# Kernel tuning notes

Measured on AMD Instinct MI355X. Metric: run time of the kernel, lower is better.

## Reference

```python
import jax, jax.numpy as jnp
import numpy as np

DIM = 2048
NH = 16
NKV = 4
HD = DIM // NH  # 128
ROPE_BASE = 10000.0
QK_GAIN_INIT = 1.0


def setup_inputs() -> dict:
    key = jax.random.key(0)
    ks = jax.random.split(key, 6)
    kv_dim = NKV * HD
    s = 0.02
    return {
        "x": jax.random.normal(ks[0], (2, 2048, DIM), dtype=jnp.float32),
        "wq": jax.random.normal(ks[1], (DIM, DIM), dtype=jnp.float32) * s,
        "wk": jax.random.normal(ks[2], (kv_dim, DIM), dtype=jnp.float32) * s,
        "wv": jax.random.normal(ks[3], (kv_dim, DIM), dtype=jnp.float32) * s,
        "wproj": jax.random.normal(ks[4], (DIM, DIM), dtype=jnp.float32) * s,
        "q_gain": jnp.full((NH,), QK_GAIN_INIT, dtype=jnp.float32),
    }


def _rms_norm(t):
    eps = jnp.asarray(jnp.finfo(t.dtype).eps, t.dtype)
    ms = jnp.mean(jnp.square(t), axis=-1, keepdims=True)
    return t * jax.lax.rsqrt(ms + eps)


def _rope_tables(seqlen, dtype):
    inv_freq = 1.0 / (ROPE_BASE ** (np.arange(0, HD, 2, dtype=np.float32) / HD))
    t = np.arange(seqlen, dtype=np.float32)
    freqs = np.outer(t, inv_freq)  # [S, HD/2]
    cos = jnp.asarray(np.cos(freqs), dtype=dtype)[None, None]  # [1,1,S,HD/2]
    sin = jnp.asarray(np.sin(freqs), dtype=dtype)[None, None]
    return cos, sin


def _apply_rotary(x, cos, sin):
    half = x.shape[-1] // 2
    x1, x2 = x[..., :half], x[..., half:]
    return jnp.concatenate((x1 * cos + x2 * sin, -x1 * sin + x2 * cos), axis=-1)


def reference(x, wq, wk, wv, wproj, q_gain):
    B, S, D = x.shape
    # projections (torch F.linear: x @ W.T), reshape to [B, H, S, HD]
    q = (x @ wq.T).reshape(B, S, NH, HD).transpose(0, 2, 1, 3)
    k = (x @ wk.T).reshape(B, S, NKV, HD).transpose(0, 2, 1, 3)
    v = (x @ wv.T).reshape(B, S, NKV, HD).transpose(0, 2, 1, 3)
    q = _rms_norm(q)
    k = _rms_norm(k)
    cos, sin = _rope_tables(S, q.dtype)
    q = _apply_rotary(q, cos, sin)
    k = _apply_rotary(k, cos, sin)
    q = q * q_gain.astype(q.dtype)[None, :, None, None]
    # GQA: expand kv heads
    G = NH // NKV
    k = jnp.repeat(k, G, axis=1)  # [B, NH, S, HD]
    v = jnp.repeat(v, G, axis=1)
    scale = 1.0 / np.sqrt(HD)
    scores = jnp.einsum("bhsd,bhtd->bhst", q, k) * scale
    causal = jnp.tril(jnp.ones((S, S), dtype=bool))
    scores = jnp.where(causal[None, None], scores, jnp.finfo(scores.dtype).min)
    attn = jax.nn.softmax(scores, axis=-1)
    y = jnp.einsum("bhst,bhtd->bhsd", attn, v)
    y = y.transpose(0, 2, 1, 3).reshape(B, S, D)
    return y @ wproj.T
```

## Files before the change

kernel.cpp:

```cpp
#include <hip/hip_runtime.h>
#include <hip/hip_bf16.h>
#include <stdint.h>

#define DIM 2048
#define NH 16
#define NKV 4
#define HD 128
#define BATCH 2
#define SEQ 2048

typedef unsigned short ushort_t;
typedef __attribute__((ext_vector_type(8))) short short8;
typedef __attribute__((ext_vector_type(4))) float f32x4;
typedef __attribute__((ext_vector_type(16))) float f32x16;

__device__ inline ushort_t f2b(float f) {
    union { float f; uint32_t u; } v; v.f = f;
    uint32_t r = (v.u + 0x7fffu + ((v.u >> 16) & 1u)) >> 16;
    return (ushort_t)r;
}

__device__ inline float fexp2(float x) {
#if __has_builtin(__builtin_amdgcn_exp2f)
    return __builtin_amdgcn_exp2f(x);
#else
    float r; asm("v_exp_f32 %0, %1" : "=v"(r) : "v"(x)); return r;
#endif
}

__device__ inline uint32_t pk2bf(float a, float b) {
    uint32_t r;
    asm("v_cvt_pk_bf16_f32 %0, %1, %2" : "=v"(r) : "v"(a), "v"(b));
    return r;
}

__global__ void cast_all(const float* __restrict__ x, const float* __restrict__ wq,
                         const float* __restrict__ wk, const float* __restrict__ wv,
                         const float* __restrict__ wp,
                         ushort_t* __restrict__ xb, ushort_t* __restrict__ wqkvb,
                         ushort_t* __restrict__ wprojb) {
    const int stride = gridDim.x * blockDim.x;
    for (int i = blockIdx.x * blockDim.x + threadIdx.x; i < 4718592; i += stride) {
        const float* s; ushort_t* d; int off;
        if (i < 2097152)      { s = x;  d = xb;               off = i; }
        else if (i < 3145728) { s = wq; d = wqkvb;            off = i - 2097152; }
        else if (i < 3407872) { s = wk; d = wqkvb + 4194304;  off = i - 3145728; }
        else if (i < 3670016) { s = wv; d = wqkvb + 5242880;  off = i - 3407872; }
        else                  { s = wp; d = wprojb;           off = i - 3670016; }
        float4 v = ((const float4*)s)[off];
        ushort4 o;
        o.x = f2b(v.x); o.y = f2b(v.y); o.z = f2b(v.z); o.w = f2b(v.w);
        ((ushort4*)d)[off] = o;
    }
}

__device__ inline void gload_lds16(const ushort_t* g, ushort_t* l) {
    __builtin_amdgcn_global_load_lds((const __attribute__((address_space(1))) void*)g,
                                     (__attribute__((address_space(3))) void*)l, 16, 0, 0);
}

__launch_bounds__(256, 2)
__global__ void gemm_bt(const ushort_t* __restrict__ A, const ushort_t* __restrict__ Bm,
                        float* __restrict__ C, int M, int N, int K) {
    __shared__ ushort_t lA[128 * 64];
    __shared__ ushort_t lB[128 * 64];
    const int t = threadIdx.x;
    const int lane = t & 63;
    const int w = t >> 6;
    const int wr = w >> 1, wc = w & 1;
    const int g = lane >> 4, l16 = lane & 15;
    const int nwg = gridDim.x * gridDim.y;
    const int bid = blockIdx.y * gridDim.x + blockIdx.x;
    const int cpx = nwg >> 3;
    const int swz = (bid & 7) * cpx + (bid >> 3);
    const int nbx = gridDim.x;
    const int m0 = (swz / nbx) * 128, n0 = (swz % nbx) * 128;

    f32x4 acc[4][4];
#pragma unroll
    for (int i = 0; i < 4; i++)
#pragma unroll
        for (int j = 0; j < 4; j++) acc[i][j] = (f32x4){0, 0, 0, 0};

    const int row_s = t >> 3;
    const int cx = t & 7;
    const int xr = (lane & 7);

    for (int kt = 0; kt < (K >> 6); ++kt) {
        const int k0 = kt * 64;
        __syncthreads();
#pragma unroll
        for (int i = 0; i < 4; i++) {
            const int ra = i * 32 + row_s;
            gload_lds16(A + (size_t)(m0 + ra) * K + k0 + ((cx ^ (row_s & 7)) * 8), lA + i * 2048 + t * 8);
            gload_lds16(Bm + (size_t)(n0 + ra) * K + k0 + ((cx ^ (row_s & 7)) * 8), lB + i * 2048 + t * 8);
        }
        __syncthreads();
#pragma unroll
        for (int kk = 0; kk < 2; kk++) {
            short8 af[4], bf[4];
#pragma unroll
            for (int i = 0; i < 4; i++) {
                af[i] = *(const short8*)(lA + (wr * 64 + i * 16 + l16) * 64 + (((kk * 4 + g) ^ xr) * 8));
                bf[i] = *(const short8*)(lB + (wc * 64 + i * 16 + l16) * 64 + (((kk * 4 + g) ^ xr) * 8));
            }
#pragma unroll
            for (int i = 0; i < 4; i++)
#pragma unroll
                for (int j = 0; j < 4; j++)
                    acc[i][j] = __builtin_amdgcn_mfma_f32_16x16x32_bf16(af[i], bf[j], acc[i][j], 0, 0, 0);
        }
    }
#pragma unroll
    for (int i = 0; i < 4; i++)
#pragma unroll
        for (int j = 0; j < 4; j++) {
            int rb = m0 + wr * 64 + i * 16 + g * 4;
            int cb = n0 + wc * 64 + j * 16 + l16;
#pragma unroll
            for (int r = 0; r < 4; r++)
                C[(size_t)(rb + r) * N + cb] = acc[i][j][r];
        }
}

__launch_bounds__(256, 2)
__global__ void gemm_qkv(const ushort_t* __restrict__ A, const ushort_t* __restrict__ Bm,
                         const float* __restrict__ qgain,
                         ushort_t* __restrict__ qb, ushort_t* __restrict__ kb,
                         ushort_t* __restrict__ vtb) {
    const int K = 2048;
    __shared__ ushort_t lA[128 * 64];
    __shared__ ushort_t lB[128 * 64];
    __shared__ float psum[2][128];
    const int t = threadIdx.x;
    const int lane = t & 63;
    const int w = t >> 6;
    const int wr = w >> 1, wc = w & 1;
    const int g = lane >> 4, l16 = lane & 15;
    const int nwg = gridDim.x * gridDim.y;
    const int bid = blockIdx.y * gridDim.x + blockIdx.x;
    const int cpx = nwg >> 3;
    const int swz = (bid & 7) * cpx + (bid >> 3);
    const int nt = swz % 24;
    const int m0 = (swz / 24) * 128, n0 = nt * 128;

    int cm[4];
    cm[0] = wc * 32 + l16;
    cm[1] = wc * 32 + 16 + l16;
    cm[2] = cm[0] + 64;
    cm[3] = cm[1] + 64;

    f32x4 acc[4][4];
#pragma unroll
    for (int i = 0; i < 4; i++)
#pragma unroll
        for (int j = 0; j < 4; j++) acc[i][j] = (f32x4){0, 0, 0, 0};

    const int row_s = t >> 3;
    const int cx = t & 7;
    const int xr = (lane & 7);

    for (int kt = 0; kt < (K >> 6); ++kt) {
        const int k0 = kt * 64;
        __syncthreads();
#pragma unroll
        for (int i = 0; i < 4; i++) {
            const int ra = i * 32 + row_s;
            gload_lds16(A + (size_t)(m0 + ra) * K + k0 + ((cx ^ (row_s & 7)) * 8), lA + i * 2048 + t * 8);
            gload_lds16(Bm + (size_t)(n0 + ra) * K + k0 + ((cx ^ (row_s & 7)) * 8), lB + i * 2048 + t * 8);
        }
        __syncthreads();
#pragma unroll
        for (int kk = 0; kk < 2; kk++) {
            short8 af[4], bf[4];
#pragma unroll
            for (int i = 0; i < 4; i++) {
                af[i] = *(const short8*)(lA + (wr * 64 + i * 16 + l16) * 64 + (((kk * 4 + g) ^ xr) * 8));
                bf[i] = *(const short8*)(lB + cm[i] * 64 + (((kk * 4 + g) ^ xr) * 8));
            }
#pragma unroll
            for (int i = 0; i < 4; i++)
#pragma unroll
                for (int j = 0; j < 4; j++)
                    acc[i][j] = __builtin_amdgcn_mfma_f32_16x16x32_bf16(af[i], bf[j], acc[i][j], 0, 0, 0);
        }
    }

    const int b = m0 >> 11;
    const int s0 = m0 & 2047;

    if (nt < 20) {
        float ssq[4][4];
#pragma unroll
        for (int i = 0; i < 4; i++)
#pragma unroll
            for (int r = 0; r < 4; r++) {
                float v = 0.0f;
#pragma unroll
                for (int j = 0; j < 4; j++) v += acc[i][j][r] * acc[i][j][r];
#pragma unroll
                for (int m = 1; m < 16; m <<= 1) v += __shfl_xor(v, m, 64);
                ssq[i][r] = v;
            }
        if (l16 == 0) {
#pragma unroll
            for (int i = 0; i < 4; i++)
#pragma unroll
                for (int r = 0; r < 4; r++)
                    psum[wc][wr * 64 + i * 16 + g * 4 + r] = ssq[i][r];
        }
        __syncthreads();

        const float gsc = (nt < 16) ? qgain[nt] * (0.08838834764831845f * 1.4426950408889634f)
                                    : 1.0f;
        ushort_t* outp = (nt < 16) ? qb + (size_t)(b * NH + nt) * SEQ * HD
                                   : kb + (size_t)(b * NKV + (nt - 16)) * SEQ * HD;
        const float inv0 = exp2f(-(float)cm[0] * (13.287712379549449f / 64.0f));
        const float inv1 = exp2f(-(float)cm[1] * (13.287712379549449f / 64.0f));
#pragma unroll
        for (int i = 0; i < 4; i++)
#pragma unroll
            for (int r = 0; r < 4; r++) {
                const int sloc = wr * 64 + i * 16 + g * 4 + r;
                const float tot = psum[0][sloc] + psum[1][sloc];
                const float rg = rsqrtf(tot * (1.0f / 128.0f) + 1.1920929e-07f) * gsc;
                const float fs = (float)(s0 + sloc);
                ushort_t* orow = outp + (size_t)(s0 + sloc) * HD;
#pragma unroll
                for (int jp = 0; jp < 2; jp++) {
                    float x1 = acc[i][jp][r], x2 = acc[i][jp + 2][r];
                    float sn, c;
                    __sincosf(fs * (jp ? inv1 : inv0), &sn, &c);
                    orow[cm[jp]]      = f2b((x1 * c + x2 * sn) * rg);
                    orow[cm[jp] + 64] = f2b((x2 * c - x1 * sn) * rg);
                }
            }
    } else {
        ushort_t* vout = vtb + (size_t)((b * NKV + (nt - 20)) * HD) * SEQ;
#pragma unroll
        for (int i = 0; i < 4; i++)
#pragma unroll
            for (int j = 0; j < 4; j++) {
                ushort4 o;
                o.x = f2b(acc[i][j][0]); o.y = f2b(acc[i][j][1]);
                o.z = f2b(acc[i][j][2]); o.w = f2b(acc[i][j][3]);
                *(ushort4*)(vout + (size_t)cm[j] * SEQ + s0 + wr * 64 + i * 16 + g * 4) = o;
            }
    }
}

#define KVB 64

__launch_bounds__(256, 2)
__global__ void attn(const ushort_t* __restrict__ qbuf, const ushort_t* __restrict__ kbuf,
                     const ushort_t* __restrict__ vtbuf, ushort_t* __restrict__ ybuf) {
    __shared__ ushort_t Klds[2][KVB * HD];
    __shared__ ushort_t Vlds[2][HD * KVB];

    const int idx = blockIdx.x;
    const int pass = idx >> 8;
    const int rr0 = idx & 255;
    const int xcd = rr0 & 7;
    const int jj = rr0 >> 5;
    const int qt = pass ? jj : 15 - jj;
    const int bh = xcd * 4 + ((rr0 >> 3) & 3);
    const int b = bh >> 4, hh = bh & 15;
    const int kvh = hh >> 2;
    const int t = threadIdx.x;
    const int w = t >> 6, lane = t & 63;
    const int l31 = lane & 31, hf = lane >> 5;
    const int q0 = qt * 128;
    const int qbase = q0 + w * 32;

    const ushort_t* Qp = qbuf + (size_t)(b * NH + hh) * SEQ * HD;
    const ushort_t* Kp = kbuf + (size_t)(b * NKV + kvh) * SEQ * HD;
    const ushort_t* Vtp = vtbuf + (size_t)(b * NKV + kvh) * HD * SEQ;

    short8 aq[8];
#pragma unroll
    for (int dc = 0; dc < 8; dc++)
        aq[dc] = *(const short8*)(Qp + (size_t)(qbase + l31) * HD + dc * 16 + hf * 8);

    f32x16 y[4];
#pragma unroll
    for (int db = 0; db < 4; db++)
#pragma unroll
        for (int r = 0; r < 16; r++) y[db][r] = 0.0f;
    float mrun = -1e30f, lrun = 0.0f;

    const int k_row = t >> 2;
    const int k_c0 = (t & 3) * 4;
    const int v_row = t >> 1;
    const int v_c0 = (t & 1) * 4;

    short8 kreg[4], vreg[4];
    const int ntiles = q0 / 64 + 2;

#pragma unroll
    for (int i = 0; i < 4; i++) {
        kreg[i] = *(const short8*)(Kp + (size_t)k_row * HD + (k_c0 + i) * 8);
        vreg[i] = *(const short8*)(Vtp + (size_t)v_row * SEQ + (v_c0 + i) * 8);
    }
    {
        ushort_t* kd = Klds[0] + k_row * HD;
        ushort_t* vd = Vlds[0] + v_row * KVB;
#pragma unroll
        for (int i = 0; i < 4; i++)
            *(short8*)(kd + (((k_c0 + i) ^ (k_row & 15)) * 8)) = kreg[i];
#pragma unroll
        for (int i = 0; i < 4; i++)
            *(short8*)(vd + (((v_c0 + i) ^ (v_row & 7)) * 8)) = vreg[i];
    }
    if (ntiles > 1) {
#pragma unroll
        for (int i = 0; i < 4; i++) {
            kreg[i] = *(const short8*)(Kp + (size_t)(KVB + k_row) * HD + (k_c0 + i) * 8);
            vreg[i] = *(const short8*)(Vtp + (size_t)v_row * SEQ + KVB + (v_c0 + i) * 8);
        }
    }
    __syncthreads();

    for (int kt = 0; kt < ntiles; ++kt) {
        const int kv0 = kt * KVB;
        if (kt + 1 < ntiles) {
            ushort_t* kd = Klds[(kt + 1) & 1] + k_row * HD;
            ushort_t* vd = Vlds[(kt + 1) & 1] + v_row * KVB;
#pragma unroll
            for (int i = 0; i < 4; i++)
                *(short8*)(kd + (((k_c0 + i) ^ (k_row & 15)) * 8)) = kreg[i];
#pragma unroll
            for (int i = 0; i < 4; i++)
                *(short8*)(vd + (((v_c0 + i) ^ (v_row & 7)) * 8)) = vreg[i];
        }
        if (kt + 2 < ntiles) {
            const int nkv0 = kv0 + 2 * KVB;
#pragma unroll
            for (int i = 0; i < 4; i++) {
                kreg[i] = *(const short8*)(Kp + (size_t)(nkv0 + k_row) * HD + (k_c0 + i) * 8);
                vreg[i] = *(const short8*)(Vtp + (size_t)v_row * SEQ + nkv0 + (v_c0 + i) * 8);
            }
        }

        if (kv0 <= qbase + 31) {
            const ushort_t* Kl = Klds[kt & 1];
            const ushort_t* Vl = Vlds[kt & 1];

            f32x16 s0v, s1v;
#pragma unroll
            for (int r = 0; r < 16; r++) { s0v[r] = 0.0f; s1v[r] = 0.0f; }
#pragma unroll
            for (int dc = 0; dc < 8; dc++) {
                short8 ak0 = *(const short8*)(Kl + (size_t)(l31) * HD      + (((dc * 2 + hf) ^ (l31 & 15)) * 8));
                short8 ak1 = *(const short8*)(Kl + (size_t)(32 + l31) * HD + (((dc * 2 + hf) ^ (l31 & 15)) * 8));
                s0v = __builtin_amdgcn_mfma_f32_32x32x16_bf16(ak0, aq[dc], s0v, 0, 0, 0);
                s1v = __builtin_amdgcn_mfma_f32_32x32x16_bf16(ak1, aq[dc], s1v, 0, 0, 0);
            }

            const int qabs = qbase + l31;
            if (kv0 + 63 > qbase) {
#pragma unroll
                for (int r = 0; r < 16; r++) {
                    int kvr = kv0 + (r & 3) + 8 * (r >> 2) + 4 * hf;
                    if (kvr > qabs)      s0v[r] = -1e30f;
                    if (kvr + 32 > qabs) s1v[r] = -1e30f;
                }
            }

            float mt = -1e30f;
#pragma unroll
            for (int r = 0; r < 16; r++) mt = fmaxf(mt, fmaxf(s0v[r], s1v[r]));
            mt = fmaxf(mt, __shfl_xor(mt, 32, 64));
            if (!__all(mt <= mrun + 8.0f)) {
                float mn = fmaxf(mrun, mt);
                float al = fexp2(mrun - mn);
                mrun = mn;
                lrun *= al;
#pragma unroll
                for (int r = 0; r < 16; r++) {
                    float alr = __shfl(al, (r & 3) + 8 * (r >> 2) + 4 * hf, 64);
#pragma unroll
                    for (int db = 0; db < 4; db++) y[db][r] *= alr;
                }
            }
            float sum = 0.0f;
#pragma unroll
            for (int r = 0; r < 16; r++) {
                float p0 = fexp2(s0v[r] - mrun);
                float p1 = fexp2(s1v[r] - mrun);
                s0v[r] = p0; s1v[r] = p1;
                sum += p0 + p1;
            }
            sum += __shfl_xor(sum, 32, 64);
            lrun += sum;

            union PW { short8 v; uint32_t wd[4]; } pa[4];
#pragma unroll
            for (int blk = 0; blk < 2; blk++) {
#pragma unroll
                for (int ks2 = 0; ks2 < 2; ks2++) {
#pragma unroll
                    for (int t2 = 0; t2 < 2; t2++) {
                        float a0 = blk ? s1v[8 * ks2 + 2 * t2]         : s0v[8 * ks2 + 2 * t2];
                        float a1 = blk ? s1v[8 * ks2 + 2 * t2 + 1]     : s0v[8 * ks2 + 2 * t2 + 1];
                        float b0 = blk ? s1v[8 * ks2 + 4 + 2 * t2]     : s0v[8 * ks2 + 4 + 2 * t2];
                        float b1 = blk ? s1v[8 * ks2 + 4 + 2 * t2 + 1] : s0v[8 * ks2 + 4 + 2 * t2 + 1];
                        uint32_t pw = pk2bf(a0, a1);
                        uint32_t qw = pk2bf(b0, b1);
                        uint32_t send = hf ? pw : qw;
                        uint32_t recv = (uint32_t)__shfl_xor((int)send, 32, 64);
                        pa[blk * 2 + ks2].wd[t2]     = hf ? recv : pw;
                        pa[blk * 2 + ks2].wd[t2 + 2] = hf ? qw : recv;
                    }
                }
            }

#pragma unroll
            for (int ks = 0; ks < 4; ks++) {
#pragma unroll
                for (int db = 0; db < 4; db++) {
                    short8 bv = *(const short8*)(Vl + (size_t)(db * 32 + l31) * KVB
                                                 + (((ks * 2 + hf) ^ (l31 & 7)) * 8));
                    y[db] = __builtin_amdgcn_mfma_f32_32x32x16_bf16(pa[ks].v, bv, y[db], 0, 0, 0);
                }
            }
        }
        __syncthreads();
    }

    float linv = 1.0f / lrun;
    ushort_t* Yp = ybuf + (size_t)b * SEQ * DIM + hh * HD;
#pragma unroll
    for (int r = 0; r < 16; r++) {
        int qloc = (r & 3) + 8 * (r >> 2) + 4 * hf;
        float lr = __shfl(linv, qloc, 64);
        int q = qbase + qloc;
#pragma unroll
        for (int db = 0; db < 4; db++)
            Yp[(size_t)q * DIM + db * 32 + l31] = f2b(y[db][r] * lr);
    }
}

extern "C" void kernel_launch(void* const* d_in, const int* in_sizes, int n_in,
                              void* d_out, int out_size, void* d_ws, size_t ws_size,
                              hipStream_t stream) {
    (void)in_sizes; (void)n_in; (void)out_size; (void)ws_size;
    const float* x     = (const float*)d_in[0];
    const float* wq    = (const float*)d_in[1];
    const float* wk    = (const float*)d_in[2];
    const float* wv    = (const float*)d_in[3];
    const float* wproj = (const float*)d_in[4];
    const float* qg    = (const float*)d_in[5];

    char* ws = (char*)d_ws;
    ushort_t* xb     = (ushort_t*)ws;
    ushort_t* wqkvb  = (ushort_t*)(ws + (16u << 20));
    ushort_t* wprojb = (ushort_t*)(ws + (28u << 20));
    ushort_t* qb     = (ushort_t*)(ws + (36u << 20));
    ushort_t* kb     = (ushort_t*)(ws + (52u << 20));
    ushort_t* vtb    = (ushort_t*)(ws + (56u << 20));
    ushort_t* yb     = (ushort_t*)(ws + (60u << 20));

    cast_all<<<2048, 256, 0, stream>>>(x, wq, wk, wv, wproj, xb, wqkvb, wprojb);
    gemm_qkv<<<dim3(24, 32), 256, 0, stream>>>(xb, wqkvb, qg, qb, kb, vtb);
    attn<<<512, 256, 0, stream>>>(qb, kb, vtb, yb);
    gemm_bt<<<dim3(16, 32), 256, 0, stream>>>(yb, wprojb, (float*)d_out, 4096, 2048, 2048);
}
```

Measured before the change: 171.0 us.

## Split long causal query tiles across two KV halves and add combine kernel

Query tiles 8–15 in the attention kernel are each split into two blocks, and each block covers half of the causal KV range. The grid grows from 512 to 768 blocks, so per-block work is more even and more blocks can run at once. Split blocks write unnormalized bf16 partial outputs plus their running max and sum to workspace, reusing the x and weight buffers that are dead by then. A new attn_combine kernel merges the two halves with log-sum-exp rescaling. The cost is an extra launch, partial-output traffic, and one more bf16 rounding of the partial results.

```diff
diff --git a/kernel.cpp b/kernel.cpp
--- a/kernel.cpp
+++ b/kernel.cpp
@@ -18,6 +18,9 @@
     union { float f; uint32_t u; } v; v.f = f;
     uint32_t r = (v.u + 0x7fffu + ((v.u >> 16) & 1u)) >> 16;
     return (ushort_t)r;
+}
+__device__ inline float b2f(ushort_t u) {
+    union { uint32_t u; float f; } v; v.u = (uint32_t)u << 16; return v.f;
 }
 
 __device__ inline float fexp2(float x) {
@@ -253,17 +256,19 @@
 
 __launch_bounds__(256, 2)
 __global__ void attn(const ushort_t* __restrict__ qbuf, const ushort_t* __restrict__ kbuf,
-                     const ushort_t* __restrict__ vtbuf, ushort_t* __restrict__ ybuf) {
+                     const ushort_t* __restrict__ vtbuf, ushort_t* __restrict__ ybuf,
+                     ushort_t* __restrict__ pY, float* __restrict__ pm, float* __restrict__ pl) {
     __shared__ ushort_t Klds[2][KVB * HD];
     __shared__ ushort_t Vlds[2][HD * KVB];
 
     const int idx = blockIdx.x;
-    const int pass = idx >> 8;
-    const int rr0 = idx & 255;
-    const int xcd = rr0 & 7;
-    const int jj = rr0 >> 5;
-    const int qt = pass ? jj : 15 - jj;
-    const int bh = xcd * 4 + ((rr0 >> 3) & 3);
+    const int xcd = idx & 7;
+    const int j = idx >> 3;
+    const int bh = xcd * 4 + (j & 3);
+    const int slot = j >> 2;
+    int qt, half, split;
+    if (slot < 16) { split = 1; qt = 8 + (slot & 7); half = slot >> 3; }
+    else           { split = 0; qt = 7 - (slot - 16); half = 0; }
     const int b = bh >> 4, hh = bh & 15;
     const int kvh = hh >> 2;
     const int t = threadIdx.x;
@@ -272,6 +277,9 @@
     const int q0 = qt * 128;
     const int qbase = q0 + w * 32;
 
+    const int kt0 = (split && half) ? qt + 1 : 0;
+    const int kt1 = split ? (half ? 2 * qt + 2 : qt + 1) : 2 * qt + 2;
+
     const ushort_t* Qp = qbuf + (size_t)(b * NH + hh) * SEQ * HD;
     const ushort_t* Kp = kbuf + (size_t)(b * NKV + kvh) * SEQ * HD;
     const ushort_t* Vtp = vtbuf + (size_t)(b * NKV + kvh) * HD * SEQ;
@@ -294,12 +302,11 @@
     const int v_c0 = (t & 1) * 4;
 
     short8 kreg[4], vreg[4];
-    const int ntiles = q0 / 64 + 2;
 
 #pragma unroll
     for (int i = 0; i < 4; i++) {
-        kreg[i] = *(const short8*)(Kp + (size_t)k_row * HD + (k_c0 + i) * 8);
-        vreg[i] = *(const short8*)(Vtp + (size_t)v_row * SEQ + (v_c0 + i) * 8);
+        kreg[i] = *(const short8*)(Kp + (size_t)(kt0 * KVB + k_row) * HD + (k_c0 + i) * 8);
+        vreg[i] = *(const short8*)(Vtp + (size_t)v_row * SEQ + kt0 * KVB + (v_c0 + i) * 8);
     }
     {
         ushort_t* kd = Klds[0] + k_row * HD;
@@ -311,20 +318,21 @@
         for (int i = 0; i < 4; i++)
             *(short8*)(vd + (((v_c0 + i) ^ (v_row & 7)) * 8)) = vreg[i];
     }
-    if (ntiles > 1) {
+    if (kt1 > kt0 + 1) {
 #pragma unroll
         for (int i = 0; i < 4; i++) {
-            kreg[i] = *(const short8*)(Kp + (size_t)(KVB + k_row) * HD + (k_c0 + i) * 8);
-            vreg[i] = *(const short8*)(Vtp + (size_t)v_row * SEQ + KVB + (v_c0 + i) * 8);
+            kreg[i] = *(const short8*)(Kp + (size_t)((kt0 + 1) * KVB + k_row) * HD + (k_c0 + i) * 8);
+            vreg[i] = *(const short8*)(Vtp + (size_t)v_row * SEQ + (kt0 + 1) * KVB + (v_c0 + i) * 8);
         }
     }
     __syncthreads();
 
-    for (int kt = 0; kt < ntiles; ++kt) {
+    for (int kt = kt0; kt < kt1; ++kt) {
+        const int it = kt - kt0;
         const int kv0 = kt * KVB;
-        if (kt + 1 < ntiles) {
-            ushort_t* kd = Klds[(kt + 1) & 1] + k_row * HD;
-            ushort_t* vd = Vlds[(kt + 1) & 1] + v_row * KVB;
+        if (kt + 1 < kt1) {
+            ushort_t* kd = Klds[(it + 1) & 1] + k_row * HD;
+            ushort_t* vd = Vlds[(it + 1) & 1] + v_row * KVB;
 #pragma unroll
             for (int i = 0; i < 4; i++)
                 *(short8*)(kd + (((k_c0 + i) ^ (k_row & 15)) * 8)) = kreg[i];
@@ -332,7 +340,7 @@
             for (int i = 0; i < 4; i++)
                 *(short8*)(vd + (((v_c0 + i) ^ (v_row & 7)) * 8)) = vreg[i];
         }
-        if (kt + 2 < ntiles) {
+        if (kt + 2 < kt1) {
             const int nkv0 = kv0 + 2 * KVB;
 #pragma unroll
             for (int i = 0; i < 4; i++) {
@@ -342,8 +350,8 @@
         }
 
         if (kv0 <= qbase + 31) {
-            const ushort_t* Kl = Klds[kt & 1];
-            const ushort_t* Vl = Vlds[kt & 1];
+            const ushort_t* Kl = Klds[it & 1];
+            const ushort_t* Vl = Vlds[it & 1];
 
             f32x16 s0v, s1v;
 #pragma unroll
@@ -427,16 +435,59 @@
         __syncthreads();
     }
 
-    float linv = 1.0f / lrun;
-    ushort_t* Yp = ybuf + (size_t)b * SEQ * DIM + hh * HD;
-#pragma unroll
-    for (int r = 0; r < 16; r++) {
-        int qloc = (r & 3) + 8 * (r >> 2) + 4 * hf;
-        float lr = __shfl(linv, qloc, 64);
-        int q = qbase + qloc;
-#pragma unroll
-        for (int db = 0; db < 4; db++)
-            Yp[(size_t)q * DIM + db * 32 + l31] = f2b(y[db][r] * lr);
+    if (!split) {
+        float linv = 1.0f / lrun;
+        ushort_t* Yp = ybuf + (size_t)b * SEQ * DIM + hh * HD;
+#pragma unroll
+        for (int r = 0; r < 16; r++) {
+            int qloc = (r & 3) + 8 * (r >> 2) + 4 * hf;
+            float lr = __shfl(linv, qloc, 64);
+            int q = qbase + qloc;
+#pragma unroll
+            for (int db = 0; db < 4; db++)
+                Yp[(size_t)q * DIM + db * 32 + l31] = f2b(y[db][r] * lr);
+        }
+    } else {
+        const int p = (((bh << 3) | (qt - 8)) << 1) | half;
+        ushort_t* Yp = pY + ((size_t)p << 14);
+#pragma unroll
+        for (int r = 0; r < 16; r++) {
+            int qloc = (r & 3) + 8 * (r >> 2) + 4 * hf;
+            int ql = w * 32 + qloc;
+#pragma unroll
+            for (int db = 0; db < 4; db++)
+                Yp[(size_t)ql * 128 + db * 32 + l31] = f2b(y[db][r]);
+        }
+        if (hf == 0) {
+            pm[p * 128 + w * 32 + l31] = mrun;
+            pl[p * 128 + w * 32 + l31] = lrun;
+        }
+    }
+}
+
+__global__ void attn_combine(const ushort_t* __restrict__ pY, const float* __restrict__ pm,
+                             const float* __restrict__ pl, ushort_t* __restrict__ ybuf) {
+    const int c = blockIdx.x;
+    const int bh = c >> 3, qto = c & 7;
+    const int b = bh >> 4, hh = bh & 15;
+    const int p0 = c << 1;
+    const ushort_t* Y0 = pY + ((size_t)p0 << 14);
+    const ushort_t* Y1 = Y0 + (1 << 14);
+    const int t = threadIdx.x;
+    const int d = t & 127, qh = t >> 7;
+    ushort_t* out = ybuf + (size_t)b * SEQ * DIM + hh * HD;
+    const int qg0 = (8 + qto) * 128;
+#pragma unroll 4
+    for (int i = 0; i < 64; i++) {
+        const int ql = i * 2 + qh;
+        float m0 = pm[p0 * 128 + ql], m1 = pm[(p0 + 1) * 128 + ql];
+        float l0 = pl[p0 * 128 + ql], l1 = pl[(p0 + 1) * 128 + ql];
+        float mx = fmaxf(m0, m1);
+        float e0 = fexp2(m0 - mx), e1 = fexp2(m1 - mx);
+        float den = e0 * l0 + e1 * l1;
+        float y0 = b2f(Y0[(size_t)ql * 128 + d]);
+        float y1 = b2f(Y1[(size_t)ql * 128 + d]);
+        out[(size_t)(qg0 + ql) * DIM + d] = f2b((e0 * y0 + e1 * y1) / den);
     }
 }
 
@@ -459,9 +510,13 @@
     ushort_t* kb     = (ushort_t*)(ws + (52u << 20));
     ushort_t* vtb    = (ushort_t*)(ws + (56u << 20));
     ushort_t* yb     = (ushort_t*)(ws + (60u << 20));
+    ushort_t* pY = (ushort_t*)ws;
+    float*    pm = (float*)(ws + (17u << 20));
+    float*    pl = (float*)(ws + (17u << 20) + (1u << 19));
 
     cast_all<<<2048, 256, 0, stream>>>(x, wq, wk, wv, wproj, xb, wqkvb, wprojb);
     gemm_qkv<<<dim3(24, 32), 256, 0, stream>>>(xb, wqkvb, qg, qb, kb, vtb);
-    attn<<<512, 256, 0, stream>>>(qb, kb, vtb, yb);
+    attn<<<768, 256, 0, stream>>>(qb, kb, vtb, yb, pY, pm, pl);
+    attn_combine<<<256, 256, 0, stream>>>(pY, pm, pl, yb);
     gemm_bt<<<dim3(16, 32), 256, 0, stream>>>(yb, wprojb, (float*)d_out, 4096, 2048, 2048);
 }
```

Measured after the change: 183.7 us. 7.4% more time.

## Double-buffer LDS tiles in projection GEMMs to overlap loads with MFMA

Applied to the files above, without the earlier changes.

Both bf16 GEMM kernels (output projection and fused QKV) now keep two LDS buffers per operand. Each iteration prefetches the next K-tile with global_load_lds before computing on the current one, and uses vmcnt waits plus raw barriers in place of the two __syncthreads per iteration. The aim is to hide global memory latency behind the MFMA work. LDS use doubles to 64KB per block, which may limit the two-blocks-per-CU occupancy target, and correctness depends on the hand-written waitcnt counts.

```diff
diff --git a/kernel.cpp b/kernel.cpp
--- a/kernel.cpp
+++ b/kernel.cpp
@@ -62,8 +62,8 @@
 __launch_bounds__(256, 2)
 __global__ void gemm_bt(const ushort_t* __restrict__ A, const ushort_t* __restrict__ Bm,
                         float* __restrict__ C, int M, int N, int K) {
-    __shared__ ushort_t lA[128 * 64];
-    __shared__ ushort_t lB[128 * 64];
+    __shared__ ushort_t lA[2][128 * 64];
+    __shared__ ushort_t lB[2][128 * 64];
     const int t = threadIdx.x;
     const int lane = t & 63;
     const int w = t >> 6;
@@ -85,24 +85,42 @@
     const int row_s = t >> 3;
     const int cx = t & 7;
     const int xr = (lane & 7);
-
-    for (int kt = 0; kt < (K >> 6); ++kt) {
-        const int k0 = kt * 64;
-        __syncthreads();
-#pragma unroll
-        for (int i = 0; i < 4; i++) {
-            const int ra = i * 32 + row_s;
-            gload_lds16(A + (size_t)(m0 + ra) * K + k0 + ((cx ^ (row_s & 7)) * 8), lA + i * 2048 + t * 8);
-            gload_lds16(Bm + (size_t)(n0 + ra) * K + k0 + ((cx ^ (row_s & 7)) * 8), lB + i * 2048 + t * 8);
-        }
-        __syncthreads();
+    const int scol = (cx ^ (row_s & 7)) * 8;
+    const int nk = K >> 6;
+
+#pragma unroll
+    for (int i = 0; i < 4; i++) {
+        const int ra = i * 32 + row_s;
+        gload_lds16(A + (size_t)(m0 + ra) * K + scol, lA[0] + i * 2048 + t * 8);
+        gload_lds16(Bm + (size_t)(n0 + ra) * K + scol, lB[0] + i * 2048 + t * 8);
+    }
+
+    for (int kt = 0; kt < nk; ++kt) {
+        if (kt + 1 < nk) {
+            const int k0n = (kt + 1) * 64;
+            ushort_t* la = lA[(kt + 1) & 1];
+            ushort_t* lb = lB[(kt + 1) & 1];
+#pragma unroll
+            for (int i = 0; i < 4; i++) {
+                const int ra = i * 32 + row_s;
+                gload_lds16(A + (size_t)(m0 + ra) * K + k0n + scol, la + i * 2048 + t * 8);
+                gload_lds16(Bm + (size_t)(n0 + ra) * K + k0n + scol, lb + i * 2048 + t * 8);
+            }
+            asm volatile("s_waitcnt vmcnt(8)" ::: "memory");
+        } else {
+            asm volatile("s_waitcnt vmcnt(0)" ::: "memory");
+        }
+        __builtin_amdgcn_s_barrier();
+
+        const ushort_t* la = lA[kt & 1];
+        const ushort_t* lb = lB[kt & 1];
 #pragma unroll
         for (int kk = 0; kk < 2; kk++) {
             short8 af[4], bf[4];
 #pragma unroll
             for (int i = 0; i < 4; i++) {
-                af[i] = *(const short8*)(lA + (wr * 64 + i * 16 + l16) * 64 + (((kk * 4 + g) ^ xr) * 8));
-                bf[i] = *(const short8*)(lB + (wc * 64 + i * 16 + l16) * 64 + (((kk * 4 + g) ^ xr) * 8));
+                af[i] = *(const short8*)(la + (wr * 64 + i * 16 + l16) * 64 + (((kk * 4 + g) ^ xr) * 8));
+                bf[i] = *(const short8*)(lb + (wc * 64 + i * 16 + l16) * 64 + (((kk * 4 + g) ^ xr) * 8));
             }
 #pragma unroll
             for (int i = 0; i < 4; i++)
@@ -110,6 +128,7 @@
                 for (int j = 0; j < 4; j++)
                     acc[i][j] = __builtin_amdgcn_mfma_f32_16x16x32_bf16(af[i], bf[j], acc[i][j], 0, 0, 0);
         }
+        __builtin_amdgcn_s_barrier();
     }
 #pragma unroll
     for (int i = 0; i < 4; i++)
@@ -129,8 +148,8 @@
                          ushort_t* __restrict__ qb, ushort_t* __restrict__ kb,
                          ushort_t* __restrict__ vtb) {
     const int K = 2048;
-    __shared__ ushort_t lA[128 * 64];
-    __shared__ ushort_t lB[128 * 64];
+    __shared__ ushort_t lA[2][128 * 64];
+    __shared__ ushort_t lB[2][128 * 64];
     __shared__ float psum[2][128];
     const int t = threadIdx.x;
     const int lane = t & 63;
@@ -159,24 +178,42 @@
     const int row_s = t >> 3;
     const int cx = t & 7;
     const int xr = (lane & 7);
-
-    for (int kt = 0; kt < (K >> 6); ++kt) {
-        const int k0 = kt * 64;
-        __syncthreads();
-#pragma unroll
-        for (int i = 0; i < 4; i++) {
-            const int ra = i * 32 + row_s;
-            gload_lds16(A + (size_t)(m0 + ra) * K + k0 + ((cx ^ (row_s & 7)) * 8), lA + i * 2048 + t * 8);
-            gload_lds16(Bm + (size_t)(n0 + ra) * K + k0 + ((cx ^ (row_s & 7)) * 8), lB + i * 2048 + t * 8);
-        }
-        __syncthreads();
+    const int scol = (cx ^ (row_s & 7)) * 8;
+    const int nk = K >> 6;
+
+#pragma unroll
+    for (int i = 0; i < 4; i++) {
+        const int ra = i * 32 + row_s;
+        gload_lds16(A + (size_t)(m0 + ra) * K + scol, lA[0] + i * 2048 + t * 8);
+        gload_lds16(Bm + (size_t)(n0 + ra) * K + scol, lB[0] + i * 2048 + t * 8);
+    }
+
+    for (int kt = 0; kt < nk; ++kt) {
+        if (kt + 1 < nk) {
+            const int k0n = (kt + 1) * 64;
+            ushort_t* la = lA[(kt + 1) & 1];
+            ushort_t* lb = lB[(kt + 1) & 1];
+#pragma unroll
+            for (int i = 0; i < 4; i++) {
+                const int ra = i * 32 + row_s;
+                gload_lds16(A + (size_t)(m0 + ra) * K + k0n + scol, la + i * 2048 + t * 8);
+                gload_lds16(Bm + (size_t)(n0 + ra) * K + k0n + scol, lb + i * 2048 + t * 8);
+            }
+            asm volatile("s_waitcnt vmcnt(8)" ::: "memory");
+        } else {
+            asm volatile("s_waitcnt vmcnt(0)" ::: "memory");
+        }
+        __builtin_amdgcn_s_barrier();
+
+        const ushort_t* la = lA[kt & 1];
+        const ushort_t* lb = lB[kt & 1];
 #pragma unroll
         for (int kk = 0; kk < 2; kk++) {
             short8 af[4], bf[4];
 #pragma unroll
             for (int i = 0; i < 4; i++) {
-                af[i] = *(const short8*)(lA + (wr * 64 + i * 16 + l16) * 64 + (((kk * 4 + g) ^ xr) * 8));
-                bf[i] = *(const short8*)(lB + cm[i] * 64 + (((kk * 4 + g) ^ xr) * 8));
+                af[i] = *(const short8*)(la + (wr * 64 + i * 16 + l16) * 64 + (((kk * 4 + g) ^ xr) * 8));
+                bf[i] = *(const short8*)(lb + cm[i] * 64 + (((kk * 4 + g) ^ xr) * 8));
             }
 #pragma unroll
             for (int i = 0; i < 4; i++)
@@ -184,6 +221,7 @@
                 for (int j = 0; j < 4; j++)
                     acc[i][j] = __builtin_amdgcn_mfma_f32_16x16x32_bf16(af[i], bf[j], acc[i][j], 0, 0, 0);
         }
+        __builtin_amdgcn_s_barrier();
     }
 
     const int b = m0 >> 11;
```

Measured after the change: 186.9 us. +9.3%, slower.
